# Optimization experiments

Measured on AMD Instinct MI355X. Metric: run time of the kernel, lower is better.

## Reference

```python
import jax, jax.numpy as jnp
import numpy as np

B_SZ, L, H, P = 16, 1024, 256, 256
DT_MIN, DT_MAX = 1e-3, 1e-1


def setup_inputs() -> dict:
    key = jax.random.key(0)
    ks = jax.random.split(key, 6)
    u = jax.random.normal(ks[0], (B_SZ, L, H), dtype=jnp.float32)
    # Stable diagonal init (stands in for HiPPO-LegS diag: negative real part,
    # spread imaginary parts) so exp(Lambda*Delta) has |.|<1 over long scans.
    Lambda_re = -0.5 * jnp.ones((P,), jnp.float32)
    Lambda_im = jnp.pi * jnp.arange(P, dtype=jnp.float32)
    Bp = jax.random.normal(ks[1], (P, H, 2), jnp.float32) / jnp.sqrt(2.0 * H)  # (P,H,2) real/imag
    Cp = jax.random.normal(ks[2], (H, P, 2), jnp.float32) / jnp.sqrt(2.0 * P)  # (H,P,2) real/imag
    D = jax.random.normal(ks[3], (H,), jnp.float32)
    log_step = (jax.random.uniform(ks[4], (P, 1), jnp.float32)
                * (jnp.log(DT_MAX) - jnp.log(DT_MIN)) + jnp.log(DT_MIN))
    return {"u": u, "Lambda_re": Lambda_re, "Lambda_im": Lambda_im,
            "B": Bp, "C": Cp, "D": D, "log_step": log_step}


def _binop(ei, ej):
    # S5 associative scan element: (A, Bu); compose linear recurrences.
    ai, bi = ei
    aj, bj = ej
    return aj * ai, aj * bi + bj


def reference(u, Lambda_re, Lambda_im, B, C, D, log_step):
    # clip_eigs=False, step_rescale=1.0, conj_sym=True, discretization='zoh'
    Lambda = Lambda_re + 1j * Lambda_im                     # (P,) complex
    B_tilde = B[..., 0] + 1j * B[..., 1]                    # (P,H) complex
    C_tilde = C[..., 0] + 1j * C[..., 1]                    # (H,P) complex
    Delta = jnp.exp(log_step[:, 0])                         # (P,)
    # ZOH discretization
    Lambda_bar = jnp.exp(Lambda * Delta)                    # (P,)
    B_bar = ((Lambda_bar - 1.0) / Lambda)[:, None] * B_tilde  # (P,H)
    # Input projection: (B, L, P) complex
    Bu = jnp.einsum('ph,blh->blp', B_bar, u.astype(B_bar.dtype))
    Lam = jnp.broadcast_to(Lambda_bar, Bu.shape)            # (B, L, P)
    # Parallel associative scan over time axis
    _, xs = jax.lax.associative_scan(_binop, (Lam, Bu), axis=1)  # states (B,L,P)
    # Output projection; conj_sym -> 2 * real part
    ys = 2.0 * jnp.einsum('hp,blp->blh', C_tilde, xs).real  # (B,L,H)
    return ys + D * u                                       # feedthrough
```

## Files before the change

### kernel.cpp

```cpp
#include <hip/hip_runtime.h>
#include <hip/hip_bf16.h>
#include <math.h>

#define BB     16
#define LSEQ   1024
#define HH     256
#define PP     256
#define MROWS  (BB*LSEQ)
#define LC     32
#define NC     (LSEQ/LC)
#define NCHUNK (BB*NC)

#define OFF_W1T  0u
#define OFF_W2T  262144u
#define OFF_CEND 524288u
#define OFF_XS   1572864u

#define XSTRIDE 520

typedef __attribute__((ext_vector_type(8))) short short8;
typedef __attribute__((ext_vector_type(4))) float floatx4;

__device__ __forceinline__ float bf2f(unsigned hs) {
    union { unsigned u; float f; } v; v.u = hs << 16; return v.f;
}
__device__ __forceinline__ unsigned short f2bs(float f) {
    __hip_bfloat16 h = __float2bfloat16(f);
    union { __hip_bfloat16 h; unsigned short s; } v; v.h = h; return v.s;
}
__device__ __forceinline__ unsigned packbf(float r, float i) {
    return (unsigned)f2bs(r) | ((unsigned)f2bs(i) << 16);
}
__device__ __forceinline__ void async16(const void* g, void* l) {
    __builtin_amdgcn_global_load_lds(
        (const __attribute__((address_space(1))) unsigned*)g,
        (__attribute__((address_space(3))) unsigned*)l, 16, 0, 0);
}
__device__ __forceinline__ float2 lam_pow(float lr, float li, float dtt) {
    float m = expf(lr * dtt);
    return make_float2(m * cosf(li * dtt), m * sinf(li * dtt));
}

__global__ void k_prep(const float* __restrict__ Bm, const float* __restrict__ Cm,
                       const float* __restrict__ Lr, const float* __restrict__ Li,
                       const float* __restrict__ ls, char* __restrict__ ws) {
    int blk = blockIdx.x, t = threadIdx.x;
    if (blk < 256) {
        int p = blk, h = t;
        float lr = Lr[p], li = Li[p];
        float dt = expf(ls[p]);
        float2 lam = lam_pow(lr, li, dt);
        float den = lr * lr + li * li;
        float nr = lam.x - 1.0f, ni = lam.y;
        float cr = (nr * lr + ni * li) / den;
        float ci = (ni * lr - nr * li) / den;
        float br = Bm[(p * HH + h) * 2 + 0];
        float bi = Bm[(p * HH + h) * 2 + 1];
        unsigned short* w1 = (unsigned short*)(ws + OFF_W1T);
        w1[(2 * p) * 256 + h]     = f2bs(cr * br - ci * bi);
        w1[(2 * p + 1) * 256 + h] = f2bs(cr * bi + ci * br);
    } else {
        int h = blk - 256, p = t;
        float c_r = Cm[(h * PP + p) * 2 + 0];
        float c_i = Cm[(h * PP + p) * 2 + 1];
        ((unsigned*)(ws + OFF_W2T))[h * 256 + p] = packbf(2.0f * c_r, -2.0f * c_i);
    }
}

__global__ __launch_bounds__(512, 4) void k_g1scan(
        const float* __restrict__ u, const float* __restrict__ Lr,
        const float* __restrict__ Li, const float* __restrict__ ls,
        char* __restrict__ ws) {
    __shared__ char smem[2048 + 33280];
    unsigned*  As32 = (unsigned*)smem;
    char*      Bs   = smem + 2048;
    unsigned short* X = (unsigned short*)(smem + 2048);
    unsigned*  X32  = (unsigned*)(smem + 2048);
    const unsigned short* W1 = (const unsigned short*)(ws + OFF_W1T);
    const int tid = threadIdx.x, bc = blockIdx.x;
    const int wave = tid >> 6, lane = tid & 63;
    const int q = lane >> 4, rr = lane & 15;
    const int c4 = lane & 3, r4 = lane >> 2;
    const int m0 = bc * LC;

    floatx4 acc[2][4];
    #pragma unroll
    for (int i = 0; i < 2; ++i)
        #pragma unroll
        for (int j = 0; j < 4; ++j) acc[i][j] = (floatx4)0.0f;

    const int urow = tid >> 4, ucol2 = (tid & 15) * 2;
    for (int k0 = 0; k0 < 256; k0 += 32) {
        __syncthreads();
        float2 v = *(const float2*)(u + (size_t)(m0 + urow) * 256 + k0 + ucol2);
        As32[urow * 16 + (tid & 15)] = packbf(v.x, v.y);
        #pragma unroll
        for (int t = wave; t < 32; t += 8)
            async16(W1 + (size_t)(t * 16 + r4) * 256 + k0 + c4 * 8,
                    Bs + t * 1024 + lane * 16);
        __syncthreads();
        short8 a0 = *(const short8*)((char*)As32 + rr * 64 + q * 16);
        short8 a1 = *(const short8*)((char*)As32 + (16 + rr) * 64 + q * 16);
        #pragma unroll
        for (int j = 0; j < 4; ++j) {
            short8 b = *(const short8*)(Bs + ((wave * 4 + j) * 16 + rr) * 64 + q * 16);
            acc[0][j] = __builtin_amdgcn_mfma_f32_16x16x32_bf16(a0, b, acc[0][j], 0, 0, 0);
            acc[1][j] = __builtin_amdgcn_mfma_f32_16x16x32_bf16(a1, b, acc[1][j], 0, 0, 0);
        }
    }
    __syncthreads();
    #pragma unroll
    for (int i = 0; i < 2; ++i)
        #pragma unroll
        for (int j = 0; j < 4; ++j)
            #pragma unroll
            for (int r0 = 0; r0 < 4; ++r0)
                X[(i * 16 + q * 4 + r0) * XSTRIDE + wave * 64 + j * 16 + rr] =
                    f2bs(acc[i][j][r0]);
    __syncthreads();

    if (tid < 256) {
        const int p = tid;
        const float2 lam = lam_pow(Lr[p], Li[p], expf(ls[p]));
        unsigned* xs32 = (unsigned*)(ws + OFF_XS);
        float xr = 0.0f, xi = 0.0f;
        for (int j = 0; j < LC; ++j) {
            unsigned cv = X32[j * (XSTRIDE / 2) + p];
            float br = bf2f(cv & 0xffffu), bi = bf2f(cv >> 16);
            float nr = fmaf(lam.x, xr, fmaf(-lam.y, xi, br));
            float ni = fmaf(lam.x, xi, fmaf(lam.y, xr, bi));
            xr = nr; xi = ni;
            xs32[(size_t)(m0 + j) * 256 + p] = packbf(xr, xi);
        }
        ((float2*)(ws + OFF_CEND))[bc * 256 + p] = make_float2(xr, xi);
    }
}

__global__ __launch_bounds__(256) void k_scanBC(
        const float* __restrict__ Lr, const float* __restrict__ Li,
        const float* __restrict__ ls, char* __restrict__ ws) {
    const int p = threadIdx.x, bc = blockIdx.x;
    const int b = bc >> 5, c = bc & (NC - 1);
    if (c == 0) return;
    const float dt = expf(ls[p]);
    const float lr = Lr[p], li = Li[p];
    const float2 lam = lam_pow(lr, li, dt);
    const float2 g = lam_pow(lr, li, dt * (float)LC);
    const float2* cend = (const float2*)(ws + OFF_CEND);

    float sr = 0.0f, si = 0.0f;
    for (int cc = 0; cc < c; ++cc) {
        float2 e = cend[(size_t)(b * NC + cc) * 256 + p];
        float nr = fmaf(g.x, sr, fmaf(-g.y, si, e.x));
        float ni = fmaf(g.x, si, fmaf(g.y, sr, e.y));
        sr = nr; si = ni;
    }

    float pr = lam.x, pi = lam.y;
    unsigned* xs32 = (unsigned*)(ws + OFF_XS);
    size_t idx = (size_t)bc * LC * 256 + p;
    for (int j = 0; j < LC; ++j) {
        float ar = pr * sr - pi * si;
        float ai = pr * si + pi * sr;
        unsigned v = xs32[idx];
        xs32[idx] = packbf(bf2f(v & 0xffffu) + ar, bf2f(v >> 16) + ai);
        float nr = pr * lam.x - pi * lam.y;
        pi = pr * lam.y + pi * lam.x; pr = nr;
        idx += 256;
    }
}

__global__ __launch_bounds__(256, 4) void k_gemm2(
        const char* __restrict__ ws_c, const float* __restrict__ D,
        const float* __restrict__ u, float* __restrict__ out) {
    __shared__ unsigned short As[64 * 32];
    __shared__ unsigned short Bs[64 * 32];
    const unsigned short* A = (const unsigned short*)(ws_c + OFF_XS);
    const unsigned short* W = (const unsigned short*)(ws_c + OFF_W2T);
    const int tid = threadIdx.x;
    const int wave = tid >> 6, lane = tid & 63;
    const int q = lane >> 4, rr = lane & 15;
    const int c4 = lane & 3, r4 = lane >> 2;
    const int wm = wave & 1, wn = wave >> 1;
    const int m0 = blockIdx.y * 64, n0 = blockIdx.x * 64;

    floatx4 acc[2][2];
    #pragma unroll
    for (int i = 0; i < 2; ++i)
        #pragma unroll
        for (int j = 0; j < 2; ++j) acc[i][j] = (floatx4)0.0f;

    for (int k0 = 0; k0 < 512; k0 += 32) {
        __syncthreads();
        async16(A + (size_t)(m0 + wave * 16 + r4) * 512 + k0 + c4 * 8,
                (char*)As + wave * 1024 + lane * 16);
        async16(W + (size_t)(n0 + wave * 16 + r4) * 512 + k0 + c4 * 8,
                (char*)Bs + wave * 1024 + lane * 16);
        __syncthreads();
        short8 a[2], b[2];
        #pragma unroll
        for (int i = 0; i < 2; ++i)
            a[i] = *(const short8*)((const char*)As + ((wm * 2 + i) * 16 + rr) * 64 + q * 16);
        #pragma unroll
        for (int j = 0; j < 2; ++j)
            b[j] = *(const short8*)((const char*)Bs + ((wn * 2 + j) * 16 + rr) * 64 + q * 16);
        #pragma unroll
        for (int i = 0; i < 2; ++i)
            #pragma unroll
            for (int j = 0; j < 2; ++j)
                acc[i][j] = __builtin_amdgcn_mfma_f32_16x16x32_bf16(a[i], b[j], acc[i][j], 0, 0, 0);
    }

    #pragma unroll
    for (int i = 0; i < 2; ++i) {
        int mbase = m0 + wm * 32 + i * 16 + q * 4;
        #pragma unroll
        for (int j = 0; j < 2; ++j) {
            int col = n0 + wn * 32 + j * 16 + rr;
            #pragma unroll
            for (int r0 = 0; r0 < 4; ++r0) {
                int row = mbase + r0;
                size_t gi = (size_t)row * 256 + col;
                out[gi] = acc[i][j][r0] + D[col] * u[gi];
            }
        }
    }
}

extern "C" void kernel_launch(void* const* d_in, const int* in_sizes, int n_in,
                              void* d_out, int out_size, void* d_ws, size_t ws_size,
                              hipStream_t stream) {
    const float* u  = (const float*)d_in[0];
    const float* Lr = (const float*)d_in[1];
    const float* Li = (const float*)d_in[2];
    const float* Bm = (const float*)d_in[3];
    const float* Cm = (const float*)d_in[4];
    const float* D  = (const float*)d_in[5];
    const float* ls = (const float*)d_in[6];
    float* out = (float*)d_out;
    char* ws = (char*)d_ws;

    k_prep<<<512, 256, 0, stream>>>(Bm, Cm, Lr, Li, ls, ws);
    k_g1scan<<<NCHUNK, 512, 0, stream>>>(u, Lr, Li, ls, ws);
    k_scanBC<<<NCHUNK, 256, 0, stream>>>(Lr, Li, ls, ws);
    k_gemm2<<<dim3(4, MROWS / 64), 256, 0, stream>>>(ws, D, u, out);
}
```

Measured before the change: 122.7 us.

## Fuse chunk carry correction into output GEMM and widen N tile

Removes the separate carry-propagation kernel that read, corrected and rewrote the full bf16 state buffer. The output GEMM block now recomputes the chunk-start carry from per-chunk end states, then applies the carry correction to the A tile while staging it into shared memory, using precomputed powers of Lambda_bar stored by the prep kernel. The GEMM N tile grows to 128 columns with a 2-wide grid, so each block recomputes the carry scan once for more output. The A tile is now loaded synchronously with VALU work instead of async loads, and every block redundantly reruns a serial carry scan of up to 31 steps.

```diff
diff --git a/kernel.cpp b/kernel.cpp
--- a/kernel.cpp
+++ b/kernel.cpp
@@ -13,8 +13,9 @@
 
 #define OFF_W1T  0u
 #define OFF_W2T  262144u
-#define OFF_CEND 524288u
-#define OFF_XS   1572864u
+#define OFF_PW   524288u
+#define OFF_CEND 655360u
+#define OFF_XS   1703936u
 
 #define XSTRIDE 520
 
@@ -59,6 +60,8 @@
         unsigned short* w1 = (unsigned short*)(ws + OFF_W1T);
         w1[(2 * p) * 256 + h]     = f2bs(cr * br - ci * bi);
         w1[(2 * p + 1) * 256 + h] = f2bs(cr * bi + ci * br);
+        if (t <= 32)
+            ((float2*)(ws + OFF_PW))[t * 256 + p] = lam_pow(lr, li, dt * (float)t);
     } else {
         int h = blk - 256, p = t;
         float c_r = Cm[(h * PP + p) * 2 + 0];
@@ -136,87 +139,101 @@
     }
 }
 
-__global__ __launch_bounds__(256) void k_scanBC(
+__global__ __launch_bounds__(256, 2) void k_gemm2fix(
+        const char* __restrict__ ws_c, const float* __restrict__ D,
+        const float* __restrict__ u, float* __restrict__ out,
         const float* __restrict__ Lr, const float* __restrict__ Li,
-        const float* __restrict__ ls, char* __restrict__ ws) {
-    const int p = threadIdx.x, bc = blockIdx.x;
-    const int b = bc >> 5, c = bc & (NC - 1);
-    if (c == 0) return;
-    const float dt = expf(ls[p]);
-    const float lr = Lr[p], li = Li[p];
-    const float2 lam = lam_pow(lr, li, dt);
-    const float2 g = lam_pow(lr, li, dt * (float)LC);
-    const float2* cend = (const float2*)(ws + OFF_CEND);
-
-    float sr = 0.0f, si = 0.0f;
-    for (int cc = 0; cc < c; ++cc) {
-        float2 e = cend[(size_t)(b * NC + cc) * 256 + p];
-        float nr = fmaf(g.x, sr, fmaf(-g.y, si, e.x));
-        float ni = fmaf(g.x, si, fmaf(g.y, sr, e.y));
-        sr = nr; si = ni;
-    }
-
-    float pr = lam.x, pi = lam.y;
-    unsigned* xs32 = (unsigned*)(ws + OFF_XS);
-    size_t idx = (size_t)bc * LC * 256 + p;
-    for (int j = 0; j < LC; ++j) {
-        float ar = pr * sr - pi * si;
-        float ai = pr * si + pi * sr;
-        unsigned v = xs32[idx];
-        xs32[idx] = packbf(bf2f(v & 0xffffu) + ar, bf2f(v >> 16) + ai);
-        float nr = pr * lam.x - pi * lam.y;
-        pi = pr * lam.y + pi * lam.x; pr = nr;
-        idx += 256;
-    }
-}
-
-__global__ __launch_bounds__(256, 4) void k_gemm2(
-        const char* __restrict__ ws_c, const float* __restrict__ D,
-        const float* __restrict__ u, float* __restrict__ out) {
+        const float* __restrict__ ls) {
     __shared__ unsigned short As[64 * 32];
-    __shared__ unsigned short Bs[64 * 32];
-    const unsigned short* A = (const unsigned short*)(ws_c + OFF_XS);
-    const unsigned short* W = (const unsigned short*)(ws_c + OFF_W2T);
+    __shared__ unsigned short Bs[128 * 32];
+    __shared__ float2 carr[2][256];
+    const unsigned short* W2 = (const unsigned short*)(ws_c + OFF_W2T);
+    const unsigned* xs32 = (const unsigned*)(ws_c + OFF_XS);
+    const float2* pw = (const float2*)(ws_c + OFF_PW);
+    const float2* cend = (const float2*)(ws_c + OFF_CEND);
+
     const int tid = threadIdx.x;
     const int wave = tid >> 6, lane = tid & 63;
     const int q = lane >> 4, rr = lane & 15;
     const int c4 = lane & 3, r4 = lane >> 2;
     const int wm = wave & 1, wn = wave >> 1;
-    const int m0 = blockIdx.y * 64, n0 = blockIdx.x * 64;
-
-    floatx4 acc[2][2];
+    const int m0 = blockIdx.y * 64, n0 = blockIdx.x * 128;
+    const int b = m0 >> 10;
+    const int c = (m0 >> 5) & 31;
+
+    {
+        const int p = tid;
+        const float dt = expf(ls[p]);
+        const float2 g = lam_pow(Lr[p], Li[p], dt * (float)LC);
+        float sr = 0.0f, si = 0.0f;
+        for (int cc = 0; cc < c; ++cc) {
+            float2 e = cend[(size_t)(b * NC + cc) * 256 + p];
+            float nr = fmaf(g.x, sr, fmaf(-g.y, si, e.x));
+            float ni = fmaf(g.x, si, fmaf(g.y, sr, e.y));
+            sr = nr; si = ni;
+        }
+        carr[0][p] = make_float2(sr, si);
+        float2 e = cend[(size_t)(b * NC + c) * 256 + p];
+        carr[1][p] = make_float2(fmaf(g.x, sr, fmaf(-g.y, si, e.x)),
+                                 fmaf(g.x, si, fmaf(g.y, sr, e.y)));
+    }
+
+    floatx4 acc[2][4];
     #pragma unroll
     for (int i = 0; i < 2; ++i)
         #pragma unroll
-        for (int j = 0; j < 2; ++j) acc[i][j] = (floatx4)0.0f;
+        for (int j = 0; j < 4; ++j) acc[i][j] = (floatx4)0.0f;
+
+    const int sr_ = tid & 63;
+    const int qd  = tid >> 6;
+    const int grow = m0 + sr_;
+    const int jj = (grow & (LC - 1)) + 1;
+    const int half = sr_ >> 5;
 
     for (int k0 = 0; k0 < 512; k0 += 32) {
         __syncthreads();
-        async16(A + (size_t)(m0 + wave * 16 + r4) * 512 + k0 + c4 * 8,
-                (char*)As + wave * 1024 + lane * 16);
-        async16(W + (size_t)(n0 + wave * 16 + r4) * 512 + k0 + c4 * 8,
-                (char*)Bs + wave * 1024 + lane * 16);
-        __syncthreads();
-        short8 a[2], b[2];
+        {
+            int p0 = (k0 >> 1) + qd * 4;
+            uint4 xv = *(const uint4*)(xs32 + (size_t)grow * 256 + p0);
+            float4 pw01 = *(const float4*)(pw + (size_t)jj * 256 + p0);
+            float4 pw23 = *(const float4*)(pw + (size_t)jj * 256 + p0 + 2);
+            float4 ca01 = *(const float4*)(&carr[half][p0]);
+            float4 ca23 = *(const float4*)(&carr[half][p0 + 2]);
+            unsigned o0 = packbf(bf2f(xv.x & 0xffffu) + (pw01.x * ca01.x - pw01.y * ca01.y),
+                                 bf2f(xv.x >> 16)     + (pw01.x * ca01.y + pw01.y * ca01.x));
+            unsigned o1 = packbf(bf2f(xv.y & 0xffffu) + (pw01.z * ca01.z - pw01.w * ca01.w),
+                                 bf2f(xv.y >> 16)     + (pw01.z * ca01.w + pw01.w * ca01.z));
+            unsigned o2 = packbf(bf2f(xv.z & 0xffffu) + (pw23.x * ca23.x - pw23.y * ca23.y),
+                                 bf2f(xv.z >> 16)     + (pw23.x * ca23.y + pw23.y * ca23.x));
+            unsigned o3 = packbf(bf2f(xv.w & 0xffffu) + (pw23.z * ca23.z - pw23.w * ca23.w),
+                                 bf2f(xv.w >> 16)     + (pw23.z * ca23.w + pw23.w * ca23.z));
+            *(uint4*)((char*)As + sr_ * 64 + qd * 16) = make_uint4(o0, o1, o2, o3);
+        }
+        #pragma unroll
+        for (int t = wave; t < 8; t += 4)
+            async16(W2 + (size_t)(n0 + t * 16 + r4) * 512 + k0 + c4 * 8,
+                    (char*)Bs + t * 1024 + lane * 16);
+        __syncthreads();
+        short8 a[2], bfrag[4];
         #pragma unroll
         for (int i = 0; i < 2; ++i)
             a[i] = *(const short8*)((const char*)As + ((wm * 2 + i) * 16 + rr) * 64 + q * 16);
         #pragma unroll
-        for (int j = 0; j < 2; ++j)
-            b[j] = *(const short8*)((const char*)Bs + ((wn * 2 + j) * 16 + rr) * 64 + q * 16);
+        for (int j = 0; j < 4; ++j)
+            bfrag[j] = *(const short8*)((const char*)Bs + ((wn * 4 + j) * 16 + rr) * 64 + q * 16);
         #pragma unroll
         for (int i = 0; i < 2; ++i)
             #pragma unroll
-            for (int j = 0; j < 2; ++j)
-                acc[i][j] = __builtin_amdgcn_mfma_f32_16x16x32_bf16(a[i], b[j], acc[i][j], 0, 0, 0);
+            for (int j = 0; j < 4; ++j)
+                acc[i][j] = __builtin_amdgcn_mfma_f32_16x16x32_bf16(a[i], bfrag[j], acc[i][j], 0, 0, 0);
     }
 
     #pragma unroll
     for (int i = 0; i < 2; ++i) {
         int mbase = m0 + wm * 32 + i * 16 + q * 4;
         #pragma unroll
-        for (int j = 0; j < 2; ++j) {
-            int col = n0 + wn * 32 + j * 16 + rr;
+        for (int j = 0; j < 4; ++j) {
+            int col = n0 + wn * 64 + j * 16 + rr;
             #pragma unroll
             for (int r0 = 0; r0 < 4; ++r0) {
                 int row = mbase + r0;
@@ -242,6 +259,5 @@
 
     k_prep<<<512, 256, 0, stream>>>(Bm, Cm, Lr, Li, ls, ws);
     k_g1scan<<<NCHUNK, 512, 0, stream>>>(u, Lr, Li, ls, ws);
-    k_scanBC<<<NCHUNK, 256, 0, stream>>>(Lr, Li, ls, ws);
-    k_gemm2<<<dim3(4, MROWS / 64), 256, 0, stream>>>(ws, D, u, out);
-}
+    k_gemm2fix<<<dim3(2, MROWS / 64), 256, 0, stream>>>(ws, D, u, out, Lr, Li, ls);
+}
```

Measured after the change: 123.2 us. No clear change (+0.4%).
